# Kernel tuning notes

Measured on AMD Instinct MI355X. Metric: run time of the kernel, lower is better.

The kernel has to match this reference:

```python
import jax, jax.numpy as jnp
import numpy as np

B, T, D, H = 2, 2048, 1024, 16
HD = D // H  # head_dim = 64


def setup_inputs() -> dict:
    key = jax.random.key(0)
    ks = jax.random.split(key, 5)
    s = 0.02
    return {
        "x": jax.random.normal(ks[0], (B, T, D), dtype=jnp.float32),
        "Wqkv": jax.random.normal(ks[1], (3 * D, D), dtype=jnp.float32) * s,
        "bqkv": jax.random.normal(ks[2], (3 * D,), dtype=jnp.float32) * s,
        "Wproj": jax.random.normal(ks[3], (D, D), dtype=jnp.float32) * s,
        "bproj": jax.random.normal(ks[4], (D,), dtype=jnp.float32) * s,
    }


def reference(x, Wqkv, bqkv, Wproj, bproj):
    b, t, d = x.shape
    qkv = x @ Wqkv.T + bqkv                      # [B,T,3D]
    q, k, v = jnp.split(qkv, 3, axis=-1)
    # [B,T,D] -> [B,H,T,HD]
    def to_heads(u):
        return u.reshape(b, t, H, HD).transpose(0, 2, 1, 3)
    q, k, v = to_heads(q), to_heads(k), to_heads(v)
    scale = 1.0 / jnp.sqrt(jnp.float32(HD))
    attn = jnp.einsum("bhqd,bhkd->bhqk", q, k) * scale   # [B,H,T,T]
    causal = jnp.tril(jnp.ones((t, t), dtype=bool))
    attn = jnp.where(causal[None, None, :, :], attn, -jnp.inf)
    attn = jax.nn.softmax(attn, axis=-1)
    scores = jnp.einsum("bhqk,bhkd->bhqd", attn, v)       # [B,H,T,HD]
    scores = scores.transpose(0, 2, 1, 3).reshape(b, t, d)
    return scores @ Wproj.T + bproj
```

## Files before the change

### kernel.cpp

```cpp
#include <hip/hip_runtime.h>

typedef __bf16 bf16_8 __attribute__((ext_vector_type(8)));
typedef __bf16 bf16_4 __attribute__((ext_vector_type(4)));
typedef __bf16 bf16_2 __attribute__((ext_vector_type(2)));
typedef float  f32_4  __attribute__((ext_vector_type(4)));
typedef float  f32_16 __attribute__((ext_vector_type(16)));

typedef __attribute__((address_space(1))) const void* as1_cvp;
typedef __attribute__((address_space(3))) void*       as3_vp;

__device__ __forceinline__ void load16_to_lds(const void* g, void* l) {
    __builtin_amdgcn_global_load_lds((as1_cvp)g, (as3_vp)l, 16, 0, 0);
}

__device__ __forceinline__ float fast_exp2(float x) {
#if __has_builtin(__builtin_amdgcn_exp2f)
    return __builtin_amdgcn_exp2f(x);
#else
    return exp2f(x);
#endif
}

__device__ __forceinline__ unsigned pk2(float lo, float hi) {
    union { bf16_2 h; unsigned u; } t;
    t.h = bf16_2{(__bf16)lo, (__bf16)hi};
    return t.u;
}

__device__ __forceinline__ void pswap(unsigned &a, unsigned &b) {
    asm("v_permlane32_swap_b32 %0, %1" : "+v"(a), "+v"(b));
}

__global__ __launch_bounds__(256) void cvt_all(
    const float* __restrict__ a, const float* __restrict__ b,
    const float* __restrict__ c, __bf16* __restrict__ out,
    int na4, int nb4, int nc4)
{
    int i = blockIdx.x * 256 + threadIdx.x;
    if (i >= na4 + nb4 + nc4) return;
    float4 f;
    if (i < na4)            f = ((const float4*)a)[i];
    else if (i < na4 + nb4) f = ((const float4*)b)[i - na4];
    else                    f = ((const float4*)c)[i - na4 - nb4];
    bf16_4 v = { (__bf16)f.x, (__bf16)f.y, (__bf16)f.z, (__bf16)f.w };
    ((bf16_4*)out)[i] = v;
}

#define BM 128

template<int OUT_BF16, int BN_, int QKV, int PIPE>
__global__ __launch_bounds__(256) void gemm_bt(
    const __bf16* __restrict__ A,
    const __bf16* __restrict__ B,
    const float*  __restrict__ bias,
    __bf16* __restrict__ Cb, float* __restrict__ Cf,
    __bf16* __restrict__ Vtb,
    int M, int N, int K, int ldc)
{
    constexpr int NT   = BN_ / 32;
    constexpr int CSTR = BN_ + (OUT_BF16 ? 8 : 4);
    constexpr int BUFB = (128 * 64 + BN_ * 64) * 2;
    constexpr int SMEMSZ = PIPE ? (3 * BUFB) : 35840;
    __shared__ __align__(16) char smem[SMEMSZ];

    const int tid  = threadIdx.x;
    const int wave = tid >> 6;
    const int lane = tid & 63;
    const int wm = wave >> 1, wn = wave & 1;
    const int quad = lane >> 4, l16 = lane & 15;
    const int bm = blockIdx.y * BM, bn = blockIdx.x * BN_;

    const int r0 = tid >> 3;
    const int ch = tid & 7;
    const int cs = (ch ^ (r0 & 7)) * 8;

    f32_4 acc[4][NT];
    #pragma unroll
    for (int i = 0; i < 4; ++i)
        #pragma unroll
        for (int j = 0; j < NT; ++j)
            acc[i][j] = f32_4{0.f, 0.f, 0.f, 0.f};

    if constexpr (!PIPE) {
        __bf16* As = (__bf16*)smem;
        __bf16* Bs = As + 128 * 64;
        for (int k0 = 0; k0 < K; k0 += 64) {
            __syncthreads();
            #pragma unroll
            for (int p = 0; p < 4; ++p) {
                int row = p * 32 + r0;
                load16_to_lds(A + (size_t)(bm + row) * K + k0 + cs,
                              &As[(p * 32 + wave * 8) * 64]);
            }
            #pragma unroll
            for (int p = 0; p < BN_ / 32; ++p) {
                int row = p * 32 + r0;
                load16_to_lds(B + (size_t)(bn + row) * K + k0 + cs,
                              &Bs[(p * 32 + wave * 8) * 64]);
            }
            __syncthreads();

            #pragma unroll
            for (int h = 0; h < 2; ++h) {
                const int sl = ((quad + h * 4) ^ (l16 & 7)) * 8;
                bf16_8 af[4], bfr[NT];
                #pragma unroll
                for (int mt = 0; mt < 4; ++mt)
                    af[mt] = *(const bf16_8*)&As[(wm * 64 + mt * 16 + l16) * 64 + sl];
                #pragma unroll
                for (int nt = 0; nt < NT; ++nt)
                    bfr[nt] = *(const bf16_8*)&Bs[(wn * (BN_/2) + nt * 16 + l16) * 64 + sl];
                #pragma unroll
                for (int mt = 0; mt < 4; ++mt)
                    #pragma unroll
                    for (int nt = 0; nt < NT; ++nt)
                        acc[mt][nt] = __builtin_amdgcn_mfma_f32_16x16x32_bf16(
                            af[mt], bfr[nt], acc[mt][nt], 0, 0, 0);
            }
        }
    } else {
        const int nit = K / 64;
        #pragma unroll
        for (int t = 0; t < 2; ++t) {
            __bf16* AsT = (__bf16*)(smem + t * BUFB);
            __bf16* BsT = AsT + 128 * 64;
            #pragma unroll
            for (int p = 0; p < 4; ++p)
                load16_to_lds(A + (size_t)(bm + p * 32 + r0) * K + t * 64 + cs,
                              &AsT[(p * 32 + wave * 8) * 64]);
            #pragma unroll
            for (int p = 0; p < BN_ / 32; ++p)
                load16_to_lds(B + (size_t)(bn + p * 32 + r0) * K + t * 64 + cs,
                              &BsT[(p * 32 + wave * 8) * 64]);
        }
        int cur = 0, sb = 2;
        for (int j = 0; j < nit; ++j) {
            if (j < nit - 1) asm volatile("s_waitcnt vmcnt(6)" ::: "memory");
            else             asm volatile("s_waitcnt vmcnt(0)" ::: "memory");
            __builtin_amdgcn_s_barrier();

            if (j + 2 < nit) {
                const int k0 = (j + 2) * 64;
                __bf16* AsT = (__bf16*)(smem + sb * BUFB);
                __bf16* BsT = AsT + 128 * 64;
                #pragma unroll
                for (int p = 0; p < 4; ++p)
                    load16_to_lds(A + (size_t)(bm + p * 32 + r0) * K + k0 + cs,
                                  &AsT[(p * 32 + wave * 8) * 64]);
                #pragma unroll
                for (int p = 0; p < BN_ / 32; ++p)
                    load16_to_lds(B + (size_t)(bn + p * 32 + r0) * K + k0 + cs,
                                  &BsT[(p * 32 + wave * 8) * 64]);
            }

            __bf16* As = (__bf16*)(smem + cur * BUFB);
            __bf16* Bs = As + 128 * 64;
            #pragma unroll
            for (int h = 0; h < 2; ++h) {
                const int sl = ((quad + h * 4) ^ (l16 & 7)) * 8;
                bf16_8 af[4], bfr[NT];
                #pragma unroll
                for (int mt = 0; mt < 4; ++mt)
                    af[mt] = *(const bf16_8*)&As[(wm * 64 + mt * 16 + l16) * 64 + sl];
                #pragma unroll
                for (int nt = 0; nt < NT; ++nt)
                    bfr[nt] = *(const bf16_8*)&Bs[(wn * (BN_/2) + nt * 16 + l16) * 64 + sl];
                #pragma unroll
                for (int mt = 0; mt < 4; ++mt)
                    #pragma unroll
                    for (int nt = 0; nt < NT; ++nt)
                        acc[mt][nt] = __builtin_amdgcn_mfma_f32_16x16x32_bf16(
                            af[mt], bfr[nt], acc[mt][nt], 0, 0, 0);
            }
            cur = (cur == 2) ? 0 : cur + 1;
            sb  = (sb  == 2) ? 0 : sb  + 1;
        }
    }

    if (QKV && bn >= 2048) {
        const int b_ = bm >> 11;
        const int t0 = (bm & 2047) + wm * 64;
        #pragma unroll
        for (int nt = 0; nt < NT; ++nt) {
            int vrow = (bn - 2048) + wn * (BN_/2) + nt * 16 + l16;
            float bv = bias ? bias[2048 + vrow] : 0.f;
            #pragma unroll
            for (int mt = 0; mt < 4; ++mt) {
                bf16_4 ov;
                #pragma unroll
                for (int r = 0; r < 4; ++r)
                    ov[r] = (__bf16)(acc[mt][nt][r] + bv);
                *(bf16_4*)(Vtb + ((size_t)b_ * 1024 + vrow) * 2048
                           + t0 + mt * 16 + quad * 4) = ov;
            }
        }
        return;
    }

    __syncthreads();

    if (OUT_BF16) {
        __bf16* Cs = (__bf16*)smem;
        #pragma unroll
        for (int mt = 0; mt < 4; ++mt)
            #pragma unroll
            for (int nt = 0; nt < NT; ++nt) {
                int col = wn * (BN_/2) + nt * 16 + l16;
                float bv = bias ? bias[bn + col] : 0.f;
                #pragma unroll
                for (int r = 0; r < 4; ++r)
                    Cs[(wm * 64 + mt * 16 + quad * 4 + r) * CSTR + col] =
                        (__bf16)(acc[mt][nt][r] + bv);
            }
        __syncthreads();
        const int rr = tid >> 4, cc = (tid & 15) * 8;
        #pragma unroll
        for (int p = 0; p < 8; ++p) {
            int row = p * 16 + rr;
            bf16_8 v = *(const bf16_8*)&Cs[row * CSTR + cc];
            *(bf16_8*)(Cb + (size_t)(bm + row) * ldc + bn + cc) = v;
        }
    } else {
        float* Cs = (float*)smem;
        #pragma unroll
        for (int mt = 0; mt < 4; ++mt)
            #pragma unroll
            for (int nt = 0; nt < NT; ++nt) {
                int col = wn * (BN_/2) + nt * 16 + l16;
                float bv = bias ? bias[bn + col] : 0.f;
                #pragma unroll
                for (int r = 0; r < 4; ++r)
                    Cs[(wm * 64 + mt * 16 + quad * 4 + r) * CSTR + col] =
                        acc[mt][nt][r] + bv;
            }
        __syncthreads();
        const int rr = tid >> 4, cc = (tid & 15) * 4;
        #pragma unroll
        for (int p = 0; p < 8; ++p) {
            int row = p * 16 + rr;
            float4 v = *(const float4*)&Cs[row * CSTR + cc];
            *(float4*)(Cf + (size_t)(bm + row) * ldc + bn + cc) = v;
        }
    }
}

__global__ __launch_bounds__(256, 2) void attn_kernel(
    const __bf16* __restrict__ qk, const __bf16* __restrict__ vt,
    __bf16* __restrict__ out)
{
    constexpr int T = 2048;
    __shared__ __align__(16) char pool[65536];
    __bf16* Ks = (__bf16*)pool;
    float*  Om = (float*)pool;
    float*  Lm = (float*)(pool + 34816);

    const int tid  = threadIdx.x;
    const int wave = tid >> 6;
    const int lane = tid & 63;
    const int wq = wave & 1, wg = wave >> 1;
    const int l32 = lane & 31, hh = lane >> 5;

    const int fid  = blockIdx.x;
    const int xcd  = fid & 7;
    const int hsel = fid >> 8;
    const int w    = (fid >> 3) & 31;
    const int qt   = hsel ? (7 - (w >> 2)) : ((w >> 2) + 8);
    const int bh   = xcd * 4 + (w & 3);
    const int b = bh >> 4, h = bh & 15;

    const size_t rowbase = (size_t)b * T;
    const __bf16* Kbase = qk + 1024 + h * 64;
    const __bf16* Vbase = vt + (size_t)bh * 64 * 2048;

    const int sr   = tid >> 3;
    const int schf = (tid & 7) ^ (sr & 7);

    constexpr float QSCALE = 0.125f * 1.4426950408889634f;
    bf16_8 aq[2][4];
    #pragma unroll
    for (int qq = 0; qq < 2; ++qq)
        #pragma unroll
        for (int df = 0; df < 4; ++df) {
            const __bf16* qp = qk + (rowbase + qt*128 + wq*64 + qq*32 + l32)*2048
                               + h*64 + df*16 + hh*8;
            bf16_8 v = *(const bf16_8*)qp;
            #pragma unroll
            for (int u = 0; u < 8; ++u) v[u] = (__bf16)((float)v[u] * QSCALE);
            aq[qq][df] = v;
        }

    #pragma unroll
    for (int sub = 0; sub < 2; ++sub)
        #pragma unroll
        for (int p = 0; p < 2; ++p) {
            load16_to_lds(Kbase + (rowbase + sub*64 + sr + 32*p)*2048 + schf*8,
                          Ks + sub*4096 + p*2048 + wave*512);
            load16_to_lds(Vbase + (size_t)(sr + 32*p)*2048 + sub*64 + schf*8,
                          Ks + 8192 + sub*4096 + p*2048 + wave*512);
        }

    f32_16 O[2][2];
    #pragma unroll
    for (int dt = 0; dt < 2; ++dt)
        #pragma unroll
        for (int qq = 0; qq < 2; ++qq)
            #pragma unroll
            for (int r = 0; r < 16; ++r) O[dt][qq][r] = 0.f;
    float l_i[2] = {0.f, 0.f};

    const int krow = wg*32 + l32;
    const int ksw  = krow & 7;

    for (int j = 0; j <= qt; ++j) {
        const int cur = j & 1, nxt = cur ^ 1;
        asm volatile("s_waitcnt vmcnt(0)" ::: "memory");
        __builtin_amdgcn_s_barrier();

        if (j < qt) {
            const int jn = j + 1;
            #pragma unroll
            for (int sub = 0; sub < 2; ++sub)
                #pragma unroll
                for (int p = 0; p < 2; ++p) {
                    load16_to_lds(Kbase + (rowbase + jn*128 + sub*64 + sr + 32*p)*2048 + schf*8,
                                  Ks + nxt*16384 + sub*4096 + p*2048 + wave*512);
                    load16_to_lds(Vbase + (size_t)(sr + 32*p)*2048 + jn*128 + sub*64 + schf*8,
                                  Ks + nxt*16384 + 8192 + sub*4096 + p*2048 + wave*512);
                }
        }

        const bool diag = (j == qt);
        #pragma unroll
        for (int s2 = 0; s2 < 2; ++s2) {
            const __bf16* Kc = Ks + cur*16384 + s2*4096;
            const __bf16* Vc = Ks + cur*16384 + 8192 + s2*4096;

            f32_16 S[2];
            __builtin_amdgcn_s_setprio(1);
            bf16_8 kf[4];
            #pragma unroll
            for (int df = 0; df < 4; ++df)
                kf[df] = *(const bf16_8*)&Kc[krow*64 + (((2*df + hh) ^ ksw) << 3)];
            #pragma unroll
            for (int qq = 0; qq < 2; ++qq) {
                f32_16 z;
                #pragma unroll
                for (int r = 0; r < 16; ++r) z[r] = 0.f;
                #pragma unroll
                for (int df = 0; df < 4; ++df)
                    z = __builtin_amdgcn_mfma_f32_32x32x16_bf16(kf[df], aq[qq][df], z, 0, 0, 0);
                S[qq] = z;
            }
            __builtin_amdgcn_s_setprio(0);

            unsigned fr[2][8];
            #pragma unroll
            for (int qq = 0; qq < 2; ++qq) {
                float pe[16];
                const int qg = qt*128 + wq*64 + qq*32 + l32;
                #pragma unroll
                for (int r = 0; r < 16; ++r) {
                    float e = fast_exp2(S[qq][r]);
                    if (diag) {
                        int key = j*128 + s2*64 + wg*32 + (r&3) + 8*(r>>2) + 4*hh;
                        if (key > qg) e = 0.f;
                    }
                    pe[r] = e;
                    l_i[qq] += e;
                }
                unsigned A = pk2(pe[0],  pe[1]),  Bv = pk2(pe[2],  pe[3]),
                         C = pk2(pe[4],  pe[5]),  D  = pk2(pe[6],  pe[7]),
                         E = pk2(pe[8],  pe[9]),  F  = pk2(pe[10], pe[11]),
                         G = pk2(pe[12], pe[13]), H  = pk2(pe[14], pe[15]);
                pswap(A, C); pswap(Bv, D); pswap(E, G); pswap(F, H);
                fr[qq][0] = A; fr[qq][1] = Bv; fr[qq][2] = C; fr[qq][3] = D;
                fr[qq][4] = E; fr[qq][5] = F;  fr[qq][6] = G; fr[qq][7] = H;
            }

            __builtin_amdgcn_s_setprio(1);
            #pragma unroll
            for (int kh = 0; kh < 2; ++kh) {
                #pragma unroll
                for (int dt = 0; dt < 2; ++dt) {
                    const int d = dt*32 + l32;
                    bf16_8 vf = *(const bf16_8*)&Vc[d*64 +
                                    (((wg*4 + kh*2 + hh) ^ (d & 7)) << 3)];
                    #pragma unroll
                    for (int qq = 0; qq < 2; ++qq) {
                        union { unsigned dw[4]; bf16_8 v; } u;
                        u.dw[0] = fr[qq][kh*4+0]; u.dw[1] = fr[qq][kh*4+1];
                        u.dw[2] = fr[qq][kh*4+2]; u.dw[3] = fr[qq][kh*4+3];
                        O[dt][qq] = __builtin_amdgcn_mfma_f32_32x32x16_bf16(
                            vf, u.v, O[dt][qq], 0, 0, 0);
                    }
                }
            }
            __builtin_amdgcn_s_setprio(0);
        }
    }

    float lw[2];
    #pragma unroll
    for (int qq = 0; qq < 2; ++qq) {
        float v = l_i[qq];
        v += __shfl_xor(v, 32, 64);
        lw[qq] = v;
    }

    __syncthreads();
    if (wg == 1) {
        #pragma unroll
        for (int qq = 0; qq < 2; ++qq) {
            const int qrow = wq*64 + qq*32 + l32;
            #pragma unroll
            for (int dt = 0; dt < 2; ++dt)
                #pragma unroll
                for (int g = 0; g < 4; ++g) {
                    f32_4 t = { O[dt][qq][g*4+0], O[dt][qq][g*4+1],
                                O[dt][qq][g*4+2], O[dt][qq][g*4+3] };
                    *(f32_4*)&Om[qrow*68 + dt*32 + g*8 + hh*4] = t;
                }
            if (hh == 0) Lm[qrow] = lw[qq];
        }
    }
    __syncthreads();
    if (wg == 0) {
        #pragma unroll
        for (int qq = 0; qq < 2; ++qq) {
            const int qrow = wq*64 + qq*32 + l32;
            const float inv = 1.f / (lw[qq] + Lm[qrow]);
            const size_t obase = (rowbase + qt*128 + qrow) * 1024 + h*64;
            #pragma unroll
            for (int dt = 0; dt < 2; ++dt)
                #pragma unroll
                for (int g = 0; g < 4; ++g) {
                    f32_4 o2 = *(const f32_4*)&Om[qrow*68 + dt*32 + g*8 + hh*4];
                    bf16_4 ov;
                    #pragma unroll
                    for (int r = 0; r < 4; ++r)
                        ov[r] = (__bf16)((O[dt][qq][g*4+r] + o2[r]) * inv);
                    *(bf16_4*)(out + obase + dt*32 + g*8 + hh*4) = ov;
                }
        }
    }
}

extern "C" void kernel_launch(void* const* d_in, const int* in_sizes, int n_in,
                              void* d_out, int out_size, void* d_ws, size_t ws_size,
                              hipStream_t stream)
{
    constexpr int Bc = 2, Tc = 2048, Dc = 1024;
    constexpr int M  = Bc * Tc;
    constexpr int N1 = 3 * Dc;

    const float* x     = (const float*)d_in[0];
    const float* Wqkv  = (const float*)d_in[1];
    const float* bqkv  = (const float*)d_in[2];
    const float* Wproj = (const float*)d_in[3];
    const float* bproj = (const float*)d_in[4];
    float* outp = (float*)d_out;

    __bf16* xb     = (__bf16*)d_ws;
    __bf16* wqkvb  = xb     + (size_t)M * Dc;
    __bf16* wprojb = wqkvb  + (size_t)N1 * Dc;
    __bf16* qkb    = wprojb + (size_t)Dc * Dc;
    __bf16* vtb    = qkb    + (size_t)M * 2048;
    __bf16* attnb  = vtb    + (size_t)Bc * 1024 * 2048;

    {
        int na4 = M * Dc / 4, nb4 = N1 * Dc / 4, nc4 = Dc * Dc / 4;
        int n4 = na4 + nb4 + nc4;
        cvt_all<<<(n4 + 255) / 256, 256, 0, stream>>>(x, Wqkv, Wproj, xb, na4, nb4, nc4);
    }

    gemm_bt<1, 128, 1, 0><<<dim3(N1 / 128, M / BM), 256, 0, stream>>>(
        xb, wqkvb, bqkv, qkb, nullptr, vtb, M, N1, Dc, 2048);

    attn_kernel<<<dim3(512), 256, 0, stream>>>(qkb, vtb, attnb);

    gemm_bt<0, 64, 0, 1><<<dim3(Dc / 64, M / BM), 256, 0, stream>>>(
        attnb, wprojb, bproj, nullptr, outp, nullptr, M, Dc, Dc, Dc);
}
```

Baseline: 160.6 us.

## Split long causal attention tiles across two blocks and merge partials

```diff
diff --git a/kernel.cpp b/kernel.cpp
--- a/kernel.cpp
+++ b/kernel.cpp
@@ -246,7 +246,8 @@
 
 __global__ __launch_bounds__(256, 2) void attn_kernel(
     const __bf16* __restrict__ qk, const __bf16* __restrict__ vt,
-    __bf16* __restrict__ out)
+    __bf16* __restrict__ out,
+    float* __restrict__ opart, float* __restrict__ lpart)
 {
     constexpr int T = 2048;
     __shared__ __align__(16) char pool[65536];
@@ -260,13 +261,29 @@
     const int wq = wave & 1, wg = wave >> 1;
     const int l32 = lane & 31, hh = lane >> 5;
 
-    const int fid  = blockIdx.x;
-    const int xcd  = fid & 7;
-    const int hsel = fid >> 8;
-    const int w    = (fid >> 3) & 31;
-    const int qt   = hsel ? (7 - (w >> 2)) : ((w >> 2) + 8);
-    const int bh   = xcd * 4 + (w & 3);
+    const int fid = blockIdx.x;
+    const int xcd = fid & 7;
+    const int u   = fid >> 3;
+    const int bh  = xcd * 4 + (u & 3);
+    const int typ = u >> 2;
     const int b = bh >> 4, h = bh & 15;
+
+    int qt, t0, t1, sidx;
+    bool direct;
+    if (typ < 16) {
+        int qa = 7 - (typ >> 1);
+        sidx = typ & 1;
+        qt = 8 + qa;
+        int half0 = (qt + 2) >> 1;
+        t0 = sidx ? half0 : 0;
+        t1 = sidx ? (qt + 1) : half0;
+        direct = false;
+    } else {
+        qt = 23 - typ;
+        sidx = 0;
+        t0 = 0; t1 = qt + 1;
+        direct = true;
+    }
 
     const size_t rowbase = (size_t)b * T;
     const __bf16* Kbase = qk + 1024 + h * 64;
@@ -285,7 +302,7 @@
                                + h*64 + df*16 + hh*8;
             bf16_8 v = *(const bf16_8*)qp;
             #pragma unroll
-            for (int u = 0; u < 8; ++u) v[u] = (__bf16)((float)v[u] * QSCALE);
+            for (int u2 = 0; u2 < 8; ++u2) v[u2] = (__bf16)((float)v[u2] * QSCALE);
             aq[qq][df] = v;
         }
 
@@ -293,9 +310,9 @@
     for (int sub = 0; sub < 2; ++sub)
         #pragma unroll
         for (int p = 0; p < 2; ++p) {
-            load16_to_lds(Kbase + (rowbase + sub*64 + sr + 32*p)*2048 + schf*8,
+            load16_to_lds(Kbase + (rowbase + t0*128 + sub*64 + sr + 32*p)*2048 + schf*8,
                           Ks + sub*4096 + p*2048 + wave*512);
-            load16_to_lds(Vbase + (size_t)(sr + 32*p)*2048 + sub*64 + schf*8,
+            load16_to_lds(Vbase + (size_t)(sr + 32*p)*2048 + t0*128 + sub*64 + schf*8,
                           Ks + 8192 + sub*4096 + p*2048 + wave*512);
         }
 
@@ -311,12 +328,12 @@
     const int krow = wg*32 + l32;
     const int ksw  = krow & 7;
 
-    for (int j = 0; j <= qt; ++j) {
-        const int cur = j & 1, nxt = cur ^ 1;
+    for (int j = t0; j < t1; ++j) {
+        const int cur = (j - t0) & 1, nxt = cur ^ 1;
         asm volatile("s_waitcnt vmcnt(0)" ::: "memory");
         __builtin_amdgcn_s_barrier();
 
-        if (j < qt) {
+        if (j + 1 < t1) {
             const int jn = j + 1;
             #pragma unroll
             for (int sub = 0; sub < 2; ++sub)
@@ -387,11 +404,11 @@
                                     (((wg*4 + kh*2 + hh) ^ (d & 7)) << 3)];
                     #pragma unroll
                     for (int qq = 0; qq < 2; ++qq) {
-                        union { unsigned dw[4]; bf16_8 v; } u;
-                        u.dw[0] = fr[qq][kh*4+0]; u.dw[1] = fr[qq][kh*4+1];
-                        u.dw[2] = fr[qq][kh*4+2]; u.dw[3] = fr[qq][kh*4+3];
+                        union { unsigned dw[4]; bf16_8 v; } u2;
+                        u2.dw[0] = fr[qq][kh*4+0]; u2.dw[1] = fr[qq][kh*4+1];
+                        u2.dw[2] = fr[qq][kh*4+2]; u2.dw[3] = fr[qq][kh*4+3];
                         O[dt][qq] = __builtin_amdgcn_mfma_f32_32x32x16_bf16(
-                            vf, u.v, O[dt][qq], 0, 0, 0);
+                            vf, u2.v, O[dt][qq], 0, 0, 0);
                     }
                 }
             }
@@ -428,20 +445,65 @@
         #pragma unroll
         for (int qq = 0; qq < 2; ++qq) {
             const int qrow = wq*64 + qq*32 + l32;
-            const float inv = 1.f / (lw[qq] + Lm[qrow]);
-            const size_t obase = (rowbase + qt*128 + qrow) * 1024 + h*64;
-            #pragma unroll
-            for (int dt = 0; dt < 2; ++dt)
-                #pragma unroll
-                for (int g = 0; g < 4; ++g) {
-                    f32_4 o2 = *(const f32_4*)&Om[qrow*68 + dt*32 + g*8 + hh*4];
-                    bf16_4 ov;
+            const float lsum = lw[qq] + Lm[qrow];
+            if (direct) {
+                const float inv = 1.f / lsum;
+                const size_t obase = (rowbase + qt*128 + qrow) * 1024 + h*64;
+                #pragma unroll
+                for (int dt = 0; dt < 2; ++dt)
                     #pragma unroll
-                    for (int r = 0; r < 4; ++r)
-                        ov[r] = (__bf16)((O[dt][qq][g*4+r] + o2[r]) * inv);
-                    *(bf16_4*)(out + obase + dt*32 + g*8 + hh*4) = ov;
-                }
-        }
+                    for (int g = 0; g < 4; ++g) {
+                        f32_4 o2 = *(const f32_4*)&Om[qrow*68 + dt*32 + g*8 + hh*4];
+                        bf16_4 ov;
+                        #pragma unroll
+                        for (int r = 0; r < 4; ++r)
+                            ov[r] = (__bf16)((O[dt][qq][g*4+r] + o2[r]) * inv);
+                        *(bf16_4*)(out + obase + dt*32 + g*8 + hh*4) = ov;
+                    }
+            } else {
+                const size_t pb = ((size_t)(bh*8 + (qt-8))*2 + sidx) * 8192
+                                  + (size_t)qrow * 64;
+                #pragma unroll
+                for (int dt = 0; dt < 2; ++dt)
+                    #pragma unroll
+                    for (int g = 0; g < 4; ++g) {
+                        f32_4 o2 = *(const f32_4*)&Om[qrow*68 + dt*32 + g*8 + hh*4];
+                        f32_4 s;
+                        #pragma unroll
+                        for (int r = 0; r < 4; ++r)
+                            s[r] = O[dt][qq][g*4+r] + o2[r];
+                        *(f32_4*)&opart[pb + dt*32 + g*8 + hh*4] = s;
+                    }
+                if (hh == 0)
+                    lpart[((bh*8 + (qt-8))*2 + sidx) * 128 + qrow] = lsum;
+            }
+        }
+    }
+}
+
+__global__ __launch_bounds__(256) void attn_merge(
+    const float* __restrict__ opart, const float* __restrict__ lpart,
+    __bf16* __restrict__ out)
+{
+    const int t  = blockIdx.x;
+    const int bh = t >> 3, qa = t & 7, qt = 8 + qa;
+    const int b = bh >> 4, h = bh & 15;
+    const int tid = threadIdx.x;
+    const int rr = tid >> 4;
+    const int cc = (tid & 15) * 4;
+    const size_t p0 = (size_t)(t*2 + 0) * 8192;
+    const size_t p1 = (size_t)(t*2 + 1) * 8192;
+    #pragma unroll
+    for (int p = 0; p < 8; ++p) {
+        const int row = p * 16 + rr;
+        const float inv = 1.f / (lpart[(t*2)*128 + row] + lpart[(t*2+1)*128 + row]);
+        f32_4 a = *(const f32_4*)&opart[p0 + row*64 + cc];
+        f32_4 c = *(const f32_4*)&opart[p1 + row*64 + cc];
+        bf16_4 ov;
+        #pragma unroll
+        for (int r = 0; r < 4; ++r)
+            ov[r] = (__bf16)((a[r] + c[r]) * inv);
+        *(bf16_4*)(out + ((size_t)b*2048 + qt*128 + row)*1024 + h*64 + cc) = ov;
     }
 }
 
@@ -466,6 +528,8 @@
     __bf16* qkb    = wprojb + (size_t)Dc * Dc;
     __bf16* vtb    = qkb    + (size_t)M * 2048;
     __bf16* attnb  = vtb    + (size_t)Bc * 1024 * 2048;
+    float*  opart  = (float*)(attnb + (size_t)M * Dc);
+    float*  lpart  = opart + (size_t)256 * 2 * 8192;
 
     {
         int na4 = M * Dc / 4, nb4 = N1 * Dc / 4, nc4 = Dc * Dc / 4;
@@ -476,7 +540,8 @@
     gemm_bt<1, 128, 1, 0><<<dim3(N1 / 128, M / BM), 256, 0, stream>>>(
         xb, wqkvb, bqkv, qkb, nullptr, vtb, M, N1, Dc, 2048);
 
-    attn_kernel<<<dim3(512), 256, 0, stream>>>(qkb, vtb, attnb);
+    attn_kernel<<<dim3(768), 256, 0, stream>>>(qkb, vtb, attnb, opart, lpart);
+    attn_merge<<<dim3(256), 256, 0, stream>>>(opart, lpart, attnb);
 
     gemm_bt<0, 64, 0, 1><<<dim3(Dc / 64, M / BM), 256, 0, stream>>>(
         attnb, wprojb, bproj, nullptr, outp, nullptr, M, Dc, Dc, Dc);
```

New measurement: 182.3 us. +13.5%, slower.
